# Performance work log

Hardware: AMD Instinct MI355X
Metric: run time of the kernel (lower is better)

The kernel has to match this reference:

```python
import jax, jax.numpy as jnp
import numpy as np
import math

B, H, S, D = 4, 8, 512, 64

def setup_inputs() -> dict:
    key = jax.random.key(0)
    k1, k2, k3, k4, k5 = jax.random.split(key, 5)
    return {
        "query": jax.random.normal(k1, (B, H, S, D), dtype=jnp.float32),
        "key": jax.random.normal(k2, (B, H, S, D), dtype=jnp.float32),
        "value": jax.random.normal(k3, (B, H, S, D), dtype=jnp.float32),
        "relem": jax.random.normal(k4, (B, S, S, D), dtype=jnp.float32),
        "mask": jax.random.randint(k5, (B, S), 0, 2, dtype=jnp.int32),
    }

def reference(query, key, value, relem, mask):
    d = query.shape[-1]
    # relscore[b,h,s,t] = sum_d q[b,h,s,d] * relem[b,s,t,d]
    relscore = jnp.einsum("bhsd,bstd->bhst", query, relem)
    scores = jnp.einsum("bhsd,bhtd->bhst", query, key)
    scores = (relscore + scores) / math.sqrt(d)
    # mask [B,S] -> [B,1,S,S] (broadcast of key mask over query positions)
    m = mask[:, None, None, :]  # repeat over query dim is a broadcast
    scores = jnp.where(m == 0, jnp.float32(-1e9), scores)
    p_attn = jax.nn.softmax(scores, axis=-1)
    ans1 = jnp.einsum("bhst,bhtd->bhsd", p_attn, value)
    ans2 = jnp.einsum("bhst,bstd->bhsd", p_attn, relem)
    return ans1 + ans2, p_attn
```

## Files before the change

### kernel.cpp

```cpp
#include <hip/hip_runtime.h>


typedef __attribute__((ext_vector_type(8))) short short8;
typedef __attribute__((ext_vector_type(4))) float f32x4;

#define MFMA16(a, b, c) __builtin_amdgcn_mfma_f32_16x16x32_bf16(a, b, c, 0, 0, 0)

__device__ __forceinline__ unsigned short f2bf(float x) {
  unsigned int u = __float_as_uint(x);
  u += 0x7fffu + ((u >> 16) & 1u);
  return (unsigned short)(u >> 16);
}
__device__ __forceinline__ float bf2f(unsigned int s) {
  return __uint_as_float(s << 16);
}
__device__ __forceinline__ short8 pack8(const float4& a, const float4& b) {
  short8 r;
  r[0] = (short)f2bf(a.x); r[1] = (short)f2bf(a.y);
  r[2] = (short)f2bf(a.z); r[3] = (short)f2bf(a.w);
  r[4] = (short)f2bf(b.x); r[5] = (short)f2bf(b.y);
  r[6] = (short)f2bf(b.z); r[7] = (short)f2bf(b.w);
  return r;
}
__device__ __forceinline__ int RLI(int t, int d) {
  return ((t << 6) | d) ^ ((((t & 7) ^ ((t >> 3) & 7))) << 3);
}
__device__ __forceinline__ int SBI(int h, int t) {
  return ((h << 9) | t) ^ ((h & 7) << 3);
}

__global__ __launch_bounds__(256, 4)
void qk_mfma(const float* __restrict__ Q, const float* __restrict__ K,
             float* __restrict__ pout) {
  const int bh   = blockIdx.x >> 6;
  const int tile = blockIdx.x & 63;
  const int s0 = (tile >> 3) << 6;
  const int t0 = (tile & 7) << 6;
  const int w    = threadIdx.x >> 6;
  const int lane = threadIdx.x & 63;
  const int rrow = lane & 15;
  const int kg   = lane >> 4;

  const float* Qb = Q + ((size_t)bh << 15);
  const float* Kb = K + ((size_t)bh << 15);

  const float* qp = Qb + (((s0 + (w << 4) + rrow) << 6) + (kg << 3));
  const short8 a0 = pack8(*reinterpret_cast<const float4*>(qp),
                          *reinterpret_cast<const float4*>(qp + 4));
  const short8 a1 = pack8(*reinterpret_cast<const float4*>(qp + 32),
                          *reinterpret_cast<const float4*>(qp + 36));

  float* pb = pout + ((size_t)bh << 18);

  float4 b0, b1, b2, b3;
  {
    const float* kp = Kb + (((t0 + rrow) << 6) + (kg << 3));
    b0 = *reinterpret_cast<const float4*>(kp);
    b1 = *reinterpret_cast<const float4*>(kp + 4);
    b2 = *reinterpret_cast<const float4*>(kp + 32);
    b3 = *reinterpret_cast<const float4*>(kp + 36);
  }
#pragma unroll
  for (int nt = 0; nt < 4; ++nt) {
    const short8 bb0 = pack8(b0, b1);
    const short8 bb1 = pack8(b2, b3);
    if (nt < 3) {
      const float* kp = Kb + (((t0 + ((nt + 1) << 4) + rrow) << 6) + (kg << 3));
      b0 = *reinterpret_cast<const float4*>(kp);
      b1 = *reinterpret_cast<const float4*>(kp + 4);
      b2 = *reinterpret_cast<const float4*>(kp + 32);
      b3 = *reinterpret_cast<const float4*>(kp + 36);
    }
    f32x4 c = {0.0f, 0.0f, 0.0f, 0.0f};
    c = MFMA16(a0, bb0, c);
    c = MFMA16(a1, bb1, c);
    const int tcol = t0 + (nt << 4) + rrow;
    const int srow = s0 + (w << 4) + (kg << 2);
#pragma unroll
    for (int r = 0; r < 4; ++r) {
      unsigned short* ob =
          reinterpret_cast<unsigned short*>(pb + ((size_t)(srow + r) << 9));
      ob[tcol] = f2bf(c[r]);
    }
  }
}

__global__ __launch_bounds__(512, 4)
void attn_v10(const float* __restrict__ Q, const float* __restrict__ R,
              const int* __restrict__ Mk, float* __restrict__ ans,
              float* __restrict__ pout) {
  __shared__ __align__(16) unsigned short smem[8 * 512 + 512 * 64];
  __shared__ __align__(16) float Pp[4][8][16];
  unsigned short* Sb = smem;
  unsigned short* Rl = smem + 8 * 512;

  const int tid = threadIdx.x;
  const int b = blockIdx.x >> 9;
  const int s = blockIdx.x & 511;
  const int bh0 = b << 3;

  const float* Rg = R + ((size_t)((b << 9) + s) << 15);

  const int d4 = tid & 15;
  const int tr = tid >> 4;

  float4 buf[8];
#pragma unroll
  for (int j = 0; j < 8; ++j)
    buf[j] = *reinterpret_cast<const float4*>(
        Rg + (((j << 5) + tr) << 6) + (d4 << 2));
#pragma unroll
  for (int j = 0; j < 8; ++j) {
    const int t = (j << 5) + tr;
    unsigned short* dst = &Rl[RLI(t, d4 << 2)];
    dst[0] = f2bf(buf[j].x); dst[1] = f2bf(buf[j].y);
    dst[2] = f2bf(buf[j].z); dst[3] = f2bf(buf[j].w);
  }
#pragma unroll
  for (int j = 0; j < 8; ++j)
    buf[j] = *reinterpret_cast<const float4*>(
        Rg + ((256 + (j << 5) + tr) << 6) + (d4 << 2));
  __syncthreads();

  const int lane = tid & 63;
  const int w    = tid >> 6;
  const int nn   = lane & 15;
  const int kg   = lane >> 4;

  float* po = pout + ((size_t)(bh0 + w) << 18) + ((size_t)s << 9);
  const unsigned short* skw = reinterpret_cast<const unsigned short*>(po);
  unsigned int skv[8];
  int mkv[8];
#pragma unroll
  for (int k = 0; k < 8; ++k) {
    skv[k] = skw[lane + (k << 6)];
    mkv[k] = Mk[(b << 9) + lane + (k << 6)];
  }

  const int hq = nn & 7;
  const float* Qg = Q + ((size_t)(((bh0 + hq) << 9) + s) << 6);
  const short8 aq0 = pack8(*reinterpret_cast<const float4*>(Qg + (kg << 3)),
                           *reinterpret_cast<const float4*>(Qg + (kg << 3) + 4));
  const short8 aq1 = pack8(*reinterpret_cast<const float4*>(Qg + 32 + (kg << 3)),
                           *reinterpret_cast<const float4*>(Qg + 36 + (kg << 3)));

#pragma unroll
  for (int i = 0; i < 2; ++i) {
    const int t0 = ((w << 1) + i) << 4;
    const short8 bb0 = *reinterpret_cast<const short8*>(&Rl[RLI(t0 + nn, kg << 3)]);
    const short8 bb1 = *reinterpret_cast<const short8*>(&Rl[RLI(t0 + nn, 32 + (kg << 3))]);
    f32x4 c = {0.0f, 0.0f, 0.0f, 0.0f};
    c = MFMA16(aq0, bb0, c);
    c = MFMA16(aq1, bb1, c);
    if (kg < 2) {
#pragma unroll
      for (int r = 0; r < 4; ++r)
        Sb[SBI((kg << 2) + r, t0 + nn)] = f2bf(c[r]);
    }
  }

#pragma unroll
  for (int j = 0; j < 8; ++j) {
    const int t = 256 + (j << 5) + tr;
    unsigned short* dst = &Rl[RLI(t, d4 << 2)];
    dst[0] = f2bf(buf[j].x); dst[1] = f2bf(buf[j].y);
    dst[2] = f2bf(buf[j].z); dst[3] = f2bf(buf[j].w);
  }
  __syncthreads();

#pragma unroll
  for (int i = 0; i < 2; ++i) {
    const int t0 = 256 + (((w << 1) + i) << 4);
    const short8 bb0 = *reinterpret_cast<const short8*>(&Rl[RLI(t0 + nn, kg << 3)]);
    const short8 bb1 = *reinterpret_cast<const short8*>(&Rl[RLI(t0 + nn, 32 + (kg << 3))]);
    f32x4 c = {0.0f, 0.0f, 0.0f, 0.0f};
    c = MFMA16(aq0, bb0, c);
    c = MFMA16(aq1, bb1, c);
    if (kg < 2) {
#pragma unroll
      for (int r = 0; r < 4; ++r)
        Sb[SBI((kg << 2) + r, t0 + nn)] = f2bf(c[r]);
    }
  }
  __syncthreads();

  {
    const int h = w;
    float v[8];
#pragma unroll
    for (int k = 0; k < 8; ++k) {
      const int t = lane + (k << 6);
      v[k] = (bf2f((unsigned int)Sb[SBI(h, t)]) + bf2f(skv[k])) * 0.125f +
             (mkv[k] ? 0.0f : -1.0e9f);
    }
    float m = v[0];
#pragma unroll
    for (int k = 1; k < 8; ++k) m = fmaxf(m, v[k]);
    m = fmaxf(m, __shfl_xor(m, 1));
    m = fmaxf(m, __shfl_xor(m, 2));
    m = fmaxf(m, __shfl_xor(m, 4));
    m = fmaxf(m, __shfl_xor(m, 8));
    m = fmaxf(m, __shfl_xor(m, 16));
    m = fmaxf(m, __shfl_xor(m, 32));

    float e[8], ss = 0.0f;
#pragma unroll
    for (int k = 0; k < 8; ++k) { e[k] = __expf(v[k] - m); ss += e[k]; }
    ss += __shfl_xor(ss, 1);
    ss += __shfl_xor(ss, 2);
    ss += __shfl_xor(ss, 4);
    ss += __shfl_xor(ss, 8);
    ss += __shfl_xor(ss, 16);
    ss += __shfl_xor(ss, 32);
    const float inv = 1.0f / ss;

#pragma unroll
    for (int k = 0; k < 8; ++k) {
      const float p = e[k] * inv;
      const int t = lane + (k << 6);
      po[t] = p;
      Sb[SBI(h, t)] = f2bf(p);
    }
  }
  __syncthreads();

  {
    const int dt = w & 3;
    const int kh = (w >> 2) & 1;
    const int n0 = dt << 4;

    f32x4 acc = {0.0f, 0.0f, 0.0f, 0.0f};
#pragma unroll
    for (int k8 = 0; k8 < 8; ++k8) {
      const int tb = (((kh << 3) + k8) << 5) + (kg << 3);
      const short8 af = *reinterpret_cast<const short8*>(&Sb[SBI(nn, tb)]);
      short8 bf;
#pragma unroll
      for (int j = 0; j < 8; ++j)
        bf[j] = (short)Rl[RLI(tb + j, n0 + nn)];
      acc = MFMA16(af, bf, acc);
    }
    if (kh == 1 && kg < 2) {
#pragma unroll
      for (int r = 0; r < 4; ++r)
        Pp[dt][(kg << 2) + r][nn] = acc[r];
    }
    __syncthreads();
    if (kh == 0 && kg < 2) {
#pragma unroll
      for (int r = 0; r < 4; ++r) {
        const int h = (kg << 2) + r;
        ans[((size_t)(((bh0 + h) << 9) + s) << 6) + n0 + nn] =
            acc[r] + Pp[dt][h][nn];
      }
    }
  }
}

__global__ __launch_bounds__(512, 4)
void pv_mfma(const float* __restrict__ V, const float* __restrict__ pout,
             float* __restrict__ ans) {
  __shared__ __align__(16) unsigned short Vl[512 * 64];

  const int tid = threadIdx.x;
  const int bh = blockIdx.x >> 4;
  const int s0 = (blockIdx.x & 15) << 5;

  const float* Vg = V + ((size_t)bh << 15);
  {
    const int d4 = tid & 15;
    const int tr = tid >> 4;
#pragma unroll
    for (int pg = 0; pg < 2; ++pg) {
      float4 tmp[8];
#pragma unroll
      for (int j = 0; j < 8; ++j) {
        const int t = (pg << 8) + (j << 5) + tr;
        tmp[j] = *reinterpret_cast<const float4*>(Vg + (t << 6) + (d4 << 2));
      }
#pragma unroll
      for (int j = 0; j < 8; ++j) {
        const int t = (pg << 8) + (j << 5) + tr;
        unsigned short* dst = &Vl[RLI(t, d4 << 2)];
        dst[0] = f2bf(tmp[j].x); dst[1] = f2bf(tmp[j].y);
        dst[2] = f2bf(tmp[j].z); dst[3] = f2bf(tmp[j].w);
      }
    }
  }
  __syncthreads();

  const int lane = tid & 63;
  const int w    = tid >> 6;
  const int nn   = lane & 15;
  const int kg   = lane >> 4;
  const int rw   = w & 1;
  const int cq   = w >> 1;
  const int n0   = cq << 4;
  const int srow = s0 + (rw << 4) + nn;

  const float* Pg = pout + ((size_t)bh << 18) + ((size_t)srow << 9);

  f32x4 acc = {0.f, 0.f, 0.f, 0.f};

  float4 pa = *reinterpret_cast<const float4*>(Pg + (kg << 3));
  float4 pb = *reinterpret_cast<const float4*>(Pg + (kg << 3) + 4);
#pragma unroll
  for (int ks = 0; ks < 16; ++ks) {
    const short8 af = pack8(pa, pb);
    if (ks < 15) {
      pa = *reinterpret_cast<const float4*>(Pg + ((ks + 1) << 5) + (kg << 3));
      pb = *reinterpret_cast<const float4*>(Pg + ((ks + 1) << 5) + (kg << 3) + 4);
    }
    const int tb = (ks << 5) + (kg << 3);
    short8 bf;
#pragma unroll
    for (int j = 0; j < 8; ++j)
      bf[j] = (short)Vl[RLI(tb + j, n0 + nn)];
    acc = MFMA16(af, bf, acc);
  }

  {
    const int sb = s0 + (rw << 4) + (kg << 2);
#pragma unroll
    for (int r = 0; r < 4; ++r) {
      float* ap = ans + ((size_t)bh << 15) + ((size_t)(sb + r) << 6) + n0 + nn;
      ap[0] += acc[r];
    }
  }
}

extern "C" void kernel_launch(void* const* d_in, const int* in_sizes, int n_in,
                              void* d_out, int out_size, void* d_ws, size_t ws_size,
                              hipStream_t stream) {
  const float* Q  = (const float*)d_in[0];
  const float* K  = (const float*)d_in[1];
  const float* V  = (const float*)d_in[2];
  const float* R  = (const float*)d_in[3];
  const int*   Mk = (const int*)d_in[4];
  float* ans  = (float*)d_out;
  float* pout = ans + (size_t)4 * 8 * 512 * 64;
  (void)d_ws; (void)ws_size; (void)in_sizes; (void)n_in; (void)out_size;

  hipLaunchKernelGGL(qk_mfma, dim3(2048), dim3(256), 0, stream, Q, K, pout);
  hipLaunchKernelGGL(attn_v10, dim3(2048), dim3(512), 0, stream,
                     Q, R, Mk, ans, pout);
  hipLaunchKernelGGL(pv_mfma, dim3(512), dim3(512), 0, stream, V, pout, ans);
}
```

Baseline: 106.1 us.

## Split relem staging into four quarters with double-buffered register prefetch

The relem tile load into LDS changes from two halves of 8 float4 per thread to four quarters of 4 float4, with two register buffers alternating. Each quarter's global load is issued before the previous quarter's MFMA score pass, so load latency overlaps compute at a finer grain and register pressure drops. The mask is also turned into an additive bias when it is loaded. The cost is two extra block-wide barriers and each wave doing one 16-row tile per quarter instead of two per half.

```diff
diff --git a/kernel.cpp b/kernel.cpp
--- a/kernel.cpp
+++ b/kernel.cpp
@@ -86,7 +86,7 @@
 }
 
 __global__ __launch_bounds__(512, 4)
-void attn_v10(const float* __restrict__ Q, const float* __restrict__ R,
+void attn_v11(const float* __restrict__ Q, const float* __restrict__ R,
               const int* __restrict__ Mk, float* __restrict__ ans,
               float* __restrict__ pout) {
   __shared__ __align__(16) unsigned short smem[8 * 512 + 512 * 64];
@@ -104,37 +104,38 @@
   const int d4 = tid & 15;
   const int tr = tid >> 4;
 
-  float4 buf[8];
-#pragma unroll
-  for (int j = 0; j < 8; ++j)
-    buf[j] = *reinterpret_cast<const float4*>(
-        Rg + (((j << 5) + tr) << 6) + (d4 << 2));
-#pragma unroll
-  for (int j = 0; j < 8; ++j) {
-    const int t = (j << 5) + tr;
-    unsigned short* dst = &Rl[RLI(t, d4 << 2)];
-    dst[0] = f2bf(buf[j].x); dst[1] = f2bf(buf[j].y);
-    dst[2] = f2bf(buf[j].z); dst[3] = f2bf(buf[j].w);
-  }
-#pragma unroll
-  for (int j = 0; j < 8; ++j)
-    buf[j] = *reinterpret_cast<const float4*>(
-        Rg + ((256 + (j << 5) + tr) << 6) + (d4 << 2));
-  __syncthreads();
-
   const int lane = tid & 63;
   const int w    = tid >> 6;
   const int nn   = lane & 15;
   const int kg   = lane >> 4;
 
+  auto LOADQ = [&](int q, float4 (&buf)[4]) {
+#pragma unroll
+    for (int j = 0; j < 4; ++j)
+      buf[j] = *reinterpret_cast<const float4*>(
+          Rg + (((q << 7) + (j << 5) + tr) << 6) + (d4 << 2));
+  };
+  auto WRITEQ = [&](int q, const float4 (&buf)[4]) {
+#pragma unroll
+    for (int j = 0; j < 4; ++j) {
+      const int t = (q << 7) + (j << 5) + tr;
+      unsigned short* dst = &Rl[RLI(t, d4 << 2)];
+      dst[0] = f2bf(buf[j].x); dst[1] = f2bf(buf[j].y);
+      dst[2] = f2bf(buf[j].z); dst[3] = f2bf(buf[j].w);
+    }
+  };
+
+  float4 bufA[4], bufB[4];
+  LOADQ(0, bufA);
+
   float* po = pout + ((size_t)(bh0 + w) << 18) + ((size_t)s << 9);
   const unsigned short* skw = reinterpret_cast<const unsigned short*>(po);
   unsigned int skv[8];
-  int mkv[8];
+  float biasv[8];
 #pragma unroll
   for (int k = 0; k < 8; ++k) {
     skv[k] = skw[lane + (k << 6)];
-    mkv[k] = Mk[(b << 9) + lane + (k << 6)];
+    biasv[k] = Mk[(b << 9) + lane + (k << 6)] ? 0.0f : -1.0e9f;
   }
 
   const int hq = nn & 7;
@@ -144,9 +145,8 @@
   const short8 aq1 = pack8(*reinterpret_cast<const float4*>(Qg + 32 + (kg << 3)),
                            *reinterpret_cast<const float4*>(Qg + 36 + (kg << 3)));
 
-#pragma unroll
-  for (int i = 0; i < 2; ++i) {
-    const int t0 = ((w << 1) + i) << 4;
+  auto RELQ = [&](int q) {
+    const int t0 = (q << 7) + (w << 4);
     const short8 bb0 = *reinterpret_cast<const short8*>(&Rl[RLI(t0 + nn, kg << 3)]);
     const short8 bb1 = *reinterpret_cast<const short8*>(&Rl[RLI(t0 + nn, 32 + (kg << 3))]);
     f32x4 c = {0.0f, 0.0f, 0.0f, 0.0f};
@@ -157,31 +157,23 @@
       for (int r = 0; r < 4; ++r)
         Sb[SBI((kg << 2) + r, t0 + nn)] = f2bf(c[r]);
     }
-  }
-
-#pragma unroll
-  for (int j = 0; j < 8; ++j) {
-    const int t = 256 + (j << 5) + tr;
-    unsigned short* dst = &Rl[RLI(t, d4 << 2)];
-    dst[0] = f2bf(buf[j].x); dst[1] = f2bf(buf[j].y);
-    dst[2] = f2bf(buf[j].z); dst[3] = f2bf(buf[j].w);
-  }
-  __syncthreads();
-
-#pragma unroll
-  for (int i = 0; i < 2; ++i) {
-    const int t0 = 256 + (((w << 1) + i) << 4);
-    const short8 bb0 = *reinterpret_cast<const short8*>(&Rl[RLI(t0 + nn, kg << 3)]);
-    const short8 bb1 = *reinterpret_cast<const short8*>(&Rl[RLI(t0 + nn, 32 + (kg << 3))]);
-    f32x4 c = {0.0f, 0.0f, 0.0f, 0.0f};
-    c = MFMA16(aq0, bb0, c);
-    c = MFMA16(aq1, bb1, c);
-    if (kg < 2) {
-#pragma unroll
-      for (int r = 0; r < 4; ++r)
-        Sb[SBI((kg << 2) + r, t0 + nn)] = f2bf(c[r]);
-    }
-  }
+  };
+
+  WRITEQ(0, bufA);
+  LOADQ(1, bufB);
+  __syncthreads();
+  RELQ(0);
+  WRITEQ(1, bufB);
+  LOADQ(2, bufA);
+  __syncthreads();
+  RELQ(1);
+  WRITEQ(2, bufA);
+  LOADQ(3, bufB);
+  __syncthreads();
+  RELQ(2);
+  WRITEQ(3, bufB);
+  __syncthreads();
+  RELQ(3);
   __syncthreads();
 
   {
@@ -191,7 +183,7 @@
     for (int k = 0; k < 8; ++k) {
       const int t = lane + (k << 6);
       v[k] = (bf2f((unsigned int)Sb[SBI(h, t)]) + bf2f(skv[k])) * 0.125f +
-             (mkv[k] ? 0.0f : -1.0e9f);
+             biasv[k];
     }
     float m = v[0];
 #pragma unroll
@@ -342,7 +334,7 @@
   (void)d_ws; (void)ws_size; (void)in_sizes; (void)n_in; (void)out_size;
 
   hipLaunchKernelGGL(qk_mfma, dim3(2048), dim3(256), 0, stream, Q, K, pout);
-  hipLaunchKernelGGL(attn_v10, dim3(2048), dim3(512), 0, stream,
+  hipLaunchKernelGGL(attn_v11, dim3(2048), dim3(512), 0, stream,
                      Q, R, Mk, ans, pout);
   hipLaunchKernelGGL(pv_mfma, dim3(512), dim3(512), 0, stream, V, pout, ans);
 }
```

After: 104.1 us (median of 2 runs). No clear change (-1.9%).
